# Optimization experiments

Measured on AMD Instinct MI355X. Metric: run time of the kernel, lower is better.

Reference implementation:

```python
import math
import jax, jax.numpy as jnp
import numpy as np

ROUTER_TEMP = 1.5
CAP_FACTOR = 1.25  # training capacity factor
NUM_EXPERTS = 16


def setup_inputs() -> dict:
    key = jax.random.key(0)
    k1, k2 = jax.random.split(key)
    N, C, H, W = 8192, 64, 8, 8
    E = NUM_EXPERTS
    X = jax.random.normal(k1, (N, C, H, W), dtype=jnp.float32)
    Wg = jax.random.normal(k2, (C, E), dtype=jnp.float32) * (1.0 / np.sqrt(C))
    bg = jnp.zeros((E,), dtype=jnp.float32)
    return {"X": X, "Wg": Wg, "bg": bg}


def reference(X, Wg, bg):
    N, C, H, W = X.shape
    E = Wg.shape[1]

    # router_gate: global average pool over (H, W) then Linear(C -> E)
    pooled = X.mean(axis=(2, 3))                       # [N, C]
    raw_logits = pooled @ Wg + bg                      # [N, E]
    logits = jnp.clip(raw_logits.astype(jnp.float32) / ROUTER_TEMP, -10.0, 10.0)
    logits_std = jnp.std(logits)

    # z-loss: mean of squared logsumexp over experts
    z_loss = jnp.mean(jnp.square(jax.nn.logsumexp(logits, axis=-1)))

    probs = jax.nn.softmax(logits, axis=1)             # [N, E]
    expert_idx = jnp.argmax(probs, axis=1)             # [N]
    expert_prob = jnp.take_along_axis(probs, expert_idx[:, None], axis=1)[:, 0]  # [N]
    expert_mask = jax.nn.one_hot(expert_idx, E, dtype=probs.dtype)               # [N, E]

    Ccap = int(max(1, math.ceil(CAP_FACTOR * N / E)))  # static capacity per expert

    # sort tokens by gate probability (descending), capacity-mask via cumsum
    order = jnp.argsort(-expert_prob)                  # [N]
    mask_sorted = expert_mask[order].astype(jnp.int32) # [N, E]
    pos_sorted = jnp.cumsum(mask_sorted, axis=0) - 1   # position within expert
    within_cap = (pos_sorted >= 0) & (pos_sorted < Ccap)
    mask_sorted = (mask_sorted.astype(bool) & within_cap).astype(jnp.int32)

    unsort = jnp.argsort(order)                        # inverse permutation
    mask = mask_sorted[unsort].astype(probs.dtype)     # [N, E]

    # aux load-balancing loss
    aux_loss = jnp.sum(mask.mean(axis=0) * probs.mean(axis=0)) * E

    # combine weights: gate prob normalized over (top-1) surviving experts
    raw = mask * expert_prob[:, None]                  # [N, E]
    denom = jax.lax.stop_gradient(jnp.clip(raw.sum(axis=1, keepdims=True), 1e-6, None))
    w = raw / denom

    pos_idx = jnp.clip(pos_sorted, 0, Ccap - 1)[unsort]          # [N, E]
    one_hot_pos = jax.nn.one_hot(pos_idx, Ccap, dtype=mask.dtype)  # [N, E, Ccap]
    combine = (w[:, :, None] * one_hot_pos).astype(X.dtype)        # [N, E, Ccap]
    dispatch = mask[:, :, None].astype(bool) & one_hot_pos.astype(bool)

    return dispatch, combine, z_loss, aux_loss, logits_std, logits
```

## Files before the change

### kernel.cpp

```cpp
#include <hip/hip_runtime.h>
#include <math.h>

#define NTOK 8192
#define NE   16
#define CAP  640
#define EC   (NE * CAP)

constexpr size_t DISP_SZ  = (size_t)NTOK * EC;
constexpr size_t SCAL_OFF = 2 * DISP_SZ;
constexpr size_t LOG_OFF  = SCAL_OFF + 3;

#define WS_KEY 0
#define WS_PD  65536
#define WS_PI  376832

#define NZBLK 5120
#define NRBLK 2048

typedef float vf4 __attribute__((ext_vector_type(4)));

__global__ __launch_bounds__(256) void k_main(
    const float4* __restrict__ X4, const float* __restrict__ Wg,
    const float* __restrict__ bg, float* __restrict__ out,
    unsigned long long* __restrict__ key,
    double* __restrict__ pD, int* __restrict__ pI)
{
    const int tid = threadIdx.x;

    if (blockIdx.x >= NRBLK) {
        vf4* o4 = (vf4*)out + (size_t)(blockIdx.x - NRBLK) * 8192;
        const vf4 z = {0.f, 0.f, 0.f, 0.f};
#pragma unroll
        for (int k = 0; k < 32; k++)
            __builtin_nontemporal_store(z, o4 + tid + 256 * k);
        return;
    }

    __shared__ double sPex[4][NE];
    __shared__ float  sLog[4][NE];
    __shared__ double sLse[4];
    __shared__ int    sExp[4];

    const int w   = tid >> 6;
    const int l   = tid & 63;
    const int n   = blockIdx.x * 4 + w;
    const int e   = l & 15;
    const int g   = l >> 4;

    float wreg[16];
#pragma unroll
    for (int i = 0; i < 16; i++)
        wreg[i] = Wg[(16 * g + i) * 16 + e];

    const float4* xb = X4 + (size_t)n * 1024;
    double dot = 0.0;
#pragma unroll
    for (int i = 0; i < 16; i++) {
        float4 v = xb[g * 256 + i * 16 + e];
        double s4 = ((double)v.x + (double)v.y) + ((double)v.z + (double)v.w);
        s4 += __shfl_xor(s4, 1, 64);
        s4 += __shfl_xor(s4, 2, 64);
        s4 += __shfl_xor(s4, 4, 64);
        s4 += __shfl_xor(s4, 8, 64);
        float pooled = (float)(s4 * (1.0 / 64.0));
        dot += (double)pooled * (double)wreg[i];
    }
    dot += __shfl_xor(dot, 16, 64);
    dot += __shfl_xor(dot, 32, 64);

    float raw = (float)dot + bg[e];
    float lg  = raw / 1.5f;
    lg = fminf(fmaxf(lg, -10.0f), 10.0f);

    float mv = lg; int mi = e;
#pragma unroll
    for (int off = 1; off <= 8; off <<= 1) {
        float ov = __shfl_xor(mv, off, 64);
        int   oi = __shfl_xor(mi, off, 64);
        if (ov > mv || (ov == mv && oi < mi)) { mv = ov; mi = oi; }
    }

    float d  = lg - mv;
    float ex = (float)exp((double)d);
    double sd = (double)ex;
#pragma unroll
    for (int off = 1; off <= 8; off <<= 1)
        sd += __shfl_xor(sd, off, 64);
    float sumf = (float)sd;
    float ptop = 1.0f / sumf;
    double lse = (double)mv + log(sd);

    unsigned int pb = __float_as_uint(ptop);
    unsigned long long kk = ((unsigned long long)mi << 43)
                          | ((unsigned long long)pb << 13)
                          | (unsigned long long)(8191 - n);

    if (l == 0) { key[n] = kk; sLse[w] = lse; sExp[w] = mi; }
    if (l < 16) {
        out[LOG_OFF + (size_t)n * 16 + e] = lg;
        sPex[w][e] = (double)ex / sd;
        sLog[w][e] = lg;
    }
    __syncthreads();

    if (tid < 16) {
        pD[blockIdx.x * 19 + 3 + tid] =
            sPex[0][tid] + sPex[1][tid] + sPex[2][tid] + sPex[3][tid];
        pI[blockIdx.x * 16 + tid] = (sExp[0] == tid) + (sExp[1] == tid)
                                  + (sExp[2] == tid) + (sExp[3] == tid);
    } else if (tid == 16) {
        double z = 0.0;
        for (int i = 0; i < 4; i++) z += sLse[i] * sLse[i];
        pD[blockIdx.x * 19 + 0] = z;
    } else if (tid == 17) {
        double s = 0.0;
        for (int i = 0; i < 4; i++)
            for (int j = 0; j < 16; j++) s += (double)sLog[i][j];
        pD[blockIdx.x * 19 + 1] = s;
    } else if (tid == 18) {
        double s = 0.0;
        for (int i = 0; i < 4; i++)
            for (int j = 0; j < 16; j++) {
                double v = (double)sLog[i][j]; s += v * v;
            }
        pD[blockIdx.x * 19 + 2] = s;
    }
}

__global__ __launch_bounds__(256) void k_scatter(
    const unsigned long long* __restrict__ key,
    const double* __restrict__ pD, const int* __restrict__ pI,
    float* __restrict__ out)
{
    __shared__ unsigned long long skey[NTOK];
    const int tid = threadIdx.x;

    if (blockIdx.x < 1024) {
        for (int k = 0; k < 32; k++)
            skey[tid + 256 * k] = key[tid + 256 * k];
        __syncthreads();

        const int tok = blockIdx.x * 8 + (tid >> 5);
        const int sub = tid & 31;
        const unsigned long long me = skey[tok];
        const unsigned long long my_e = me >> 43;

        int cnt = 0;
        for (int m = sub; m < NTOK; m += 32) {
            unsigned long long km = skey[m];
            cnt += ((km >> 43) == my_e && km > me) ? 1 : 0;
        }
#pragma unroll
        for (int off = 16; off >= 1; off >>= 1)
            cnt += __shfl_down(cnt, off, 32);

        if (sub == 0 && cnt < CAP) {
            size_t idx = (size_t)tok * EC + (size_t)my_e * CAP + (size_t)cnt;
            __builtin_nontemporal_store(1.0f, out + idx);
            __builtin_nontemporal_store(1.0f, out + DISP_SZ + idx);
        }
        return;
    }

    double* sD = (double*)skey;
    int*    sI = (int*)(skey + 5120);
    double a[19];
#pragma unroll
    for (int f = 0; f < 19; f++) a[f] = 0.0;
    int ci[NE];
#pragma unroll
    for (int f = 0; f < NE; f++) ci[f] = 0;

    for (int b = tid; b < 2048; b += 256) {
        const double* rowD = pD + b * 19;
#pragma unroll
        for (int f = 0; f < 19; f++) a[f] += rowD[f];
        const int* rowI = pI + b * NE;
#pragma unroll
        for (int f = 0; f < NE; f++) ci[f] += rowI[f];
    }
#pragma unroll
    for (int f = 0; f < 19; f++) sD[tid * 20 + f] = a[f];
#pragma unroll
    for (int f = 0; f < NE; f++) sI[tid * 16 + f] = ci[f];
    __syncthreads();

    if (tid == 0) {
        double tot[19];
        for (int f = 0; f < 19; f++) tot[f] = 0.0;
        int totI[NE];
        for (int f = 0; f < NE; f++) totI[f] = 0;
        for (int i = 0; i < 256; i++) {
            for (int f = 0; f < 19; f++) tot[f] += sD[i * 20 + f];
            for (int f = 0; f < NE; f++) totI[f] += sI[i * 16 + f];
        }
        double z = tot[0] / (double)NTOK;
        double aux = 0.0;
        for (int e = 0; e < NE; e++) {
            int kept = totI[e] < CAP ? totI[e] : CAP;
            aux += ((double)kept / (double)NTOK) * (tot[3 + e] / (double)NTOK);
        }
        aux *= (double)NE;
        double cntall = (double)NTOK * NE;
        double mean = tot[1] / cntall;
        double var  = tot[2] / cntall - mean * mean;
        if (var < 0.0) var = 0.0;
        out[SCAL_OFF + 0] = (float)z;
        out[SCAL_OFF + 1] = (float)aux;
        out[SCAL_OFF + 2] = (float)sqrt(var);
    }
}

extern "C" void kernel_launch(void* const* d_in, const int* in_sizes, int n_in,
                              void* d_out, int out_size, void* d_ws, size_t ws_size,
                              hipStream_t stream)
{
    const float* X  = (const float*)d_in[0];
    const float* Wg = (const float*)d_in[1];
    const float* bg = (const float*)d_in[2];
    float* out = (float*)d_out;

    char* ws = (char*)d_ws;
    unsigned long long* key = (unsigned long long*)(ws + WS_KEY);
    double* pD = (double*)(ws + WS_PD);
    int*    pI = (int*)   (ws + WS_PI);

    k_main<<<NRBLK + NZBLK, 256, 0, stream>>>((const float4*)X, Wg, bg, out,
                                              key, pD, pI);
    k_scatter<<<1025, 256, 0, stream>>>(key, pD, pI, out);
}
```

Baseline: 822.2 us.

## Fuse output zero-fill with dispatch/combine scatter into single write pass

Removes the separate zero-fill blocks from the router kernel and has each scatter block write the full dispatch and combine rows for its eight tokens, embedding the single 1.0 in the zero vector. This avoids writing the large output twice (zero then scatter), and also unrolls the rank-counting loop and vectorizes the key load into shared memory. The trade-off is that the output writes now wait until routing finishes instead of overlapping with it, and they use regular rather than nontemporal stores.

After: 805.4 us. -2.0%, faster.

```diff
diff --git a/kernel.cpp b/kernel.cpp
--- a/kernel.cpp
+++ b/kernel.cpp
@@ -7,6 +7,7 @@
 #define EC   (NE * CAP)
 
 constexpr size_t DISP_SZ  = (size_t)NTOK * EC;
+constexpr size_t DISP4    = DISP_SZ / 4;
 constexpr size_t SCAL_OFF = 2 * DISP_SZ;
 constexpr size_t LOG_OFF  = SCAL_OFF + 3;
 
@@ -14,27 +15,17 @@
 #define WS_PD  65536
 #define WS_PI  376832
 
-#define NZBLK 5120
 #define NRBLK 2048
 
 typedef float vf4 __attribute__((ext_vector_type(4)));
 
-__global__ __launch_bounds__(256) void k_main(
+__global__ __launch_bounds__(256) void k_router(
     const float4* __restrict__ X4, const float* __restrict__ Wg,
     const float* __restrict__ bg, float* __restrict__ out,
     unsigned long long* __restrict__ key,
     double* __restrict__ pD, int* __restrict__ pI)
 {
     const int tid = threadIdx.x;
-
-    if (blockIdx.x >= NRBLK) {
-        vf4* o4 = (vf4*)out + (size_t)(blockIdx.x - NRBLK) * 8192;
-        const vf4 z = {0.f, 0.f, 0.f, 0.f};
-#pragma unroll
-        for (int k = 0; k < 32; k++)
-            __builtin_nontemporal_store(z, o4 + tid + 256 * k);
-        return;
-    }
 
     __shared__ double sPex[4][NE];
     __shared__ float  sLog[4][NE];
@@ -127,37 +118,72 @@
     }
 }
 
-__global__ __launch_bounds__(256) void k_scatter(
+__global__ __launch_bounds__(256) void k_write(
     const unsigned long long* __restrict__ key,
     const double* __restrict__ pD, const int* __restrict__ pI,
     float* __restrict__ out)
 {
     __shared__ unsigned long long skey[NTOK];
+    __shared__ int sFid[8];
     const int tid = threadIdx.x;
 
     if (blockIdx.x < 1024) {
-        for (int k = 0; k < 32; k++)
-            skey[tid + 256 * k] = key[tid + 256 * k];
+        {
+            const ulonglong2* kp = (const ulonglong2*)key;
+            ulonglong2* sp = (ulonglong2*)skey;
+#pragma unroll
+            for (int k = 0; k < 16; k++)
+                sp[tid + 256 * k] = kp[tid + 256 * k];
+        }
         __syncthreads();
 
-        const int tok = blockIdx.x * 8 + (tid >> 5);
+        const int grp = tid >> 5;
         const int sub = tid & 31;
-        const unsigned long long me = skey[tok];
+        const int tok = blockIdx.x * 8 + grp;
+        const unsigned long long me   = skey[tok];
         const unsigned long long my_e = me >> 43;
 
-        int cnt = 0;
-        for (int m = sub; m < NTOK; m += 32) {
-            unsigned long long km = skey[m];
-            cnt += ((km >> 43) == my_e && km > me) ? 1 : 0;
-        }
+        int c0 = 0, c1 = 0, c2 = 0, c3 = 0;
+        for (int m = sub; m < NTOK; m += 128) {
+            unsigned long long k0 = skey[m];
+            unsigned long long k1 = skey[m + 32];
+            unsigned long long k2 = skey[m + 64];
+            unsigned long long k3 = skey[m + 96];
+            c0 += ((k0 >> 43) == my_e && k0 > me) ? 1 : 0;
+            c1 += ((k1 >> 43) == my_e && k1 > me) ? 1 : 0;
+            c2 += ((k2 >> 43) == my_e && k2 > me) ? 1 : 0;
+            c3 += ((k3 >> 43) == my_e && k3 > me) ? 1 : 0;
+        }
+        int cnt = (c0 + c1) + (c2 + c3);
 #pragma unroll
         for (int off = 16; off >= 1; off >>= 1)
             cnt += __shfl_down(cnt, off, 32);
 
-        if (sub == 0 && cnt < CAP) {
-            size_t idx = (size_t)tok * EC + (size_t)my_e * CAP + (size_t)cnt;
-            __builtin_nontemporal_store(1.0f, out + idx);
-            __builtin_nontemporal_store(1.0f, out + DISP_SZ + idx);
+        if (sub == 0)
+            sFid[grp] = (cnt < CAP) ? (int)(my_e * CAP + (unsigned long long)cnt)
+                                    : -1;
+        __syncthreads();
+
+        vf4* o4 = (vf4*)out;
+#pragma unroll
+        for (int j = 0; j < 8; j++) {
+            const size_t base = (size_t)(blockIdx.x * 8 + j) * (EC / 4);
+            const int fid  = sFid[j];
+            const int f4   = fid >> 2;
+            const int comp = fid & 3;
+#pragma unroll
+            for (int k = 0; k < 10; k++) {
+                const int p = tid + 256 * k;
+                vf4 z = {0.f, 0.f, 0.f, 0.f};
+                if (p == f4) {
+                    if      (comp == 0) z.x = 1.0f;
+                    else if (comp == 1) z.y = 1.0f;
+                    else if (comp == 2) z.z = 1.0f;
+                    else                z.w = 1.0f;
+                }
+                o4[base + p]         = z;
+                o4[DISP4 + base + p] = z;
+            }
         }
         return;
     }
@@ -225,7 +251,7 @@
     double* pD = (double*)(ws + WS_PD);
     int*    pI = (int*)   (ws + WS_PI);
 
-    k_main<<<NRBLK + NZBLK, 256, 0, stream>>>((const float4*)X, Wg, bg, out,
-                                              key, pD, pI);
-    k_scatter<<<1025, 256, 0, stream>>>(key, pD, pI, out);
+    k_router<<<NRBLK, 256, 0, stream>>>((const float4*)X, Wg, bg, out,
+                                        key, pD, pI);
+    k_write<<<1025, 256, 0, stream>>>(key, pD, pI, out);
 }
```
